# Optimization experiments

Hardware: AMD Instinct MI355X
Metric: run time of the kernel (lower is better)

## Reference

```python
import jax, jax.numpy as jnp
import numpy as np
import math

# dims (see shape_source)
B, S, D, H, DH, W, L, F = 2, 4096, 768, 12, 64, 256, 4, 2048
DV, DID, NIN, V, CD, CS = 256, 32, 8, 4, 16, 64
DEMB = CD * CS
EPS = 1e-6
NEG = -1e9


def rmsnorm(x, w):
    y = x * jax.lax.rsqrt(jnp.mean(x * x, axis=-1, keepdims=True) + EPS)
    return y * w


def sliding_attn(q, k, v):
    # q,k,v: [B,H,S,DH]; banded attention, each query attends keys within +-W.
    nc = S // W
    q = q * (1.0 / math.sqrt(DH))
    kp = jnp.pad(k, ((0, 0), (0, 0), (W, W), (0, 0)))
    vp = jnp.pad(v, ((0, 0), (0, 0), (W, W), (0, 0)))
    idx = jnp.arange(nc)[:, None] * W + jnp.arange(3 * W)[None, :]  # [nc,3W] into padded seq
    kc = kp[:, :, idx]                                # [B,H,nc,3W,DH]
    vc = vp[:, :, idx]
    qc = q.reshape(B, H, nc, W, DH)
    scores = jnp.einsum('bhcqd,bhckd->bhcqk', qc, kc)  # [B,H,nc,W,3W]
    qpos = jnp.arange(W)[:, None]
    kpos = jnp.arange(3 * W)[None, :]
    band = jnp.abs(kpos - (qpos + W)) <= W             # [W,3W]
    kglob = jnp.arange(nc)[:, None, None] * W + kpos[None] - W  # [nc,1,3W]
    valid = band[None] & (kglob >= 0) & (kglob < S)    # [nc,W,3W]
    scores = jnp.where(valid[None, None], scores, NEG)
    probs = jax.nn.softmax(scores, axis=-1)
    out = jnp.einsum('bhcqk,bhckd->bhcqd', probs, vc)
    return out.reshape(B, H, S, DH)


def _forward(x, id, embed_table, cd_w, cd_b, wq, bq, wk, bk, wv, bv,
             attn_norm_w, ffn_norm_w, w1, b1, w2, b2, w3, b3,
             h0_w1, h0_b1, h0_w2, h0_b2, norm_head0_w, head0_w, head0_b,
             c1_w1, c1_b1, c1_w2, c1_b2, c2_w1, c2_b1, c2_w2, c2_b2,
             norm_emb_w, head1_w, head1_b):
    h = embed_table[x] * math.sqrt(DV)                         # [B,S,DV]
    bits = jnp.arange(DID - 1, -1, -1)
    idb = ((id[..., None] >> bits) & 1).astype(jnp.float32)    # decimal2binary -> [B,S,DID]
    h = jnp.concatenate([h, idb], axis=-1) @ cd_w + cd_b       # correct_dim -> [B,S,D]
    for l in range(L):
        a = rmsnorm(h, attn_norm_w[l])
        q = (a @ wq[l] + bq[l]).reshape(B, S, H, DH).transpose(0, 2, 1, 3)
        k = (a @ wk[l] + bk[l]).reshape(B, S, H, DH).transpose(0, 2, 1, 3)
        v = (a @ wv[l] + bv[l]).reshape(B, S, H, DH).transpose(0, 2, 1, 3)
        o = sliding_attn(q, k, v)                              # [B,H,S,DH]
        h = h + o.transpose(0, 2, 1, 3).reshape(B, S, D)
        f = rmsnorm(h, ffn_norm_w[l])
        h = h + (jax.nn.silu(f @ w1[l] + b1[l]) * (f @ w3[l] + b3[l])) @ w2[l] + b2[l]
    # per-token head
    t = jax.nn.silu(h @ h0_w1 + h0_b1) @ h0_w2 + h0_b2
    logits0 = rmsnorm(t, norm_head0_w) @ head0_w + head0_b     # [B,S,V]
    # compression head
    c = jax.nn.silu(h @ c1_w1 + c1_b1) @ c1_w2 + c1_b2         # [B,S,CD]
    c = c.transpose(0, 2, 1)                                    # [B,CD,S]
    c = jax.nn.silu(c @ c2_w1 + c2_b1) @ c2_w2 + c2_b2         # [B,CD,CS]
    c = c.transpose(0, 2, 1).reshape(B, DEMB)
    emb = rmsnorm(c, norm_emb_w)
    logits = (emb @ head1_w + head1_b).reshape(B, S, V)        # [B,S,V]
    return logits0, logits


def setup_inputs() -> dict:
    key = jax.random.key(0)
    ks = iter(jax.random.split(key, 80))
    def w(*shape):
        return jax.random.normal(next(ks), shape, jnp.float32) * 0.02
    z = lambda *shape: jnp.zeros(shape, jnp.float32)
    o = lambda *shape: jnp.ones(shape, jnp.float32)
    return {
        'x': jax.random.randint(next(ks), (B, S), 0, NIN),
        'id': jax.random.randint(next(ks), (B, S), 0, 2 ** 20),
        'embed_table': w(NIN, DV),
        'cd_w': w(DV + DID, D), 'cd_b': z(D),
        'wq': w(L, D, D), 'bq': z(L, D),
        'wk': w(L, D, D), 'bk': z(L, D),
        'wv': w(L, D, D), 'bv': z(L, D),
        'attn_norm_w': o(L, D), 'ffn_norm_w': o(L, D),
        'w1': w(L, D, F), 'b1': z(L, F),
        'w2': w(L, F, D), 'b2': z(L, D),
        'w3': w(L, D, F), 'b3': z(L, F),
        'h0_w1': w(D, D), 'h0_b1': z(D),
        'h0_w2': w(D, D), 'h0_b2': z(D),
        'norm_head0_w': o(D),
        'head0_w': w(D, V), 'head0_b': z(V),
        'c1_w1': w(D, D), 'c1_b1': z(D),
        'c1_w2': w(D, CD), 'c1_b2': z(CD),
        'c2_w1': w(S, S), 'c2_b1': z(S),
        'c2_w2': w(S, CS), 'c2_b2': z(CS),
        'norm_emb_w': o(DEMB),
        'head1_w': w(DEMB, S * V), 'head1_b': z(S * V),
    }


def reference(x, id, embed_table, cd_w, cd_b, wq, bq, wk, bk, wv, bv,
              attn_norm_w, ffn_norm_w, w1, b1, w2, b2, w3, b3,
              h0_w1, h0_b1, h0_w2, h0_b2, norm_head0_w, head0_w, head0_b,
              c1_w1, c1_b1, c1_w2, c1_b2, c2_w1, c2_b1, c2_w2, c2_b2,
              norm_emb_w, head1_w, head1_b):
    return _forward(x, id, embed_table, cd_w, cd_b, wq, bq, wk, bk, wv, bv,
                    attn_norm_w, ffn_norm_w, w1, b1, w2, b2, w3, b3,
                    h0_w1, h0_b1, h0_w2, h0_b2, norm_head0_w, head0_w, head0_b,
                    c1_w1, c1_b1, c1_w2, c1_b2, c2_w1, c2_b1, c2_w2, c2_b2,
                    norm_emb_w, head1_w, head1_b)
```

## Files before the change

kernel.cpp:

```cpp
#include <hip/hip_runtime.h>
#include <stdint.h>

typedef unsigned short u16;
typedef unsigned int u32;

#define SS 4096
#define NROWS 8192

__device__ __forceinline__ float bf2f(u16 u){
  union { u32 u; float f; } x; x.u = ((u32)u) << 16; return x.f;
}
__device__ __forceinline__ u16 f2bf(float f){
  union { float f; u32 u; } x; x.f = f;
  u32 r = x.u + 0x7fffu + ((x.u >> 16) & 1u);
  return (u16)(r >> 16);
}
__device__ __forceinline__ float bflo(u32 u){ union { u32 u; float f; } x; x.u = u << 16; return x.f; }
__device__ __forceinline__ float bfhi(u32 u){ union { u32 u; float f; } x; x.u = u & 0xffff0000u; return x.f; }

__device__ __forceinline__ float ldany(const void* p, size_t i, int f){
  return f ? ((const float*)p)[i] : bf2f(((const u16*)p)[i]);
}

__global__ void detect_k(const void* anw, int* flag){
  if (threadIdx.x == 0 && blockIdx.x == 0)
    flag[0] = (((const u32*)anw)[0] == 0x3F800000u) ? 1 : 0;
}

__device__ __forceinline__ void gload16(const u16* g, u16* l){
  __builtin_amdgcn_global_load_lds((const __attribute__((address_space(1))) void*)g,
                                   (__attribute__((address_space(3))) void*)l, 16, 0, 0);
}

typedef __attribute__((ext_vector_type(8))) __bf16 bf16x8;
typedef __attribute__((ext_vector_type(4))) float f32x4;

__device__ __forceinline__ bf16x8 ldsr16(const u16* p){
  bf16x8 r;
  u32 a = (u32)(uintptr_t)(const __attribute__((address_space(3))) u16*)p;
  asm volatile("ds_read_b128 %0, %1" : "=v"(r) : "v"(a));
  return r;
}

__global__ void transpose_k(const void* __restrict__ in, size_t ioff,
                            u16* __restrict__ out, int R, int C, const int* fl){
  int f = *fl;
  __shared__ u16 t[32][33];
  int c0 = blockIdx.x * 32, r0 = blockIdx.y * 32;
  int tx = threadIdx.x & 31, ty = threadIdx.x >> 5;
  #pragma unroll
  for (int i = 0; i < 32; i += 8){
    int r = r0 + ty + i, c = c0 + tx;
    t[ty + i][tx] = (r < R && c < C) ? f2bf(ldany(in, ioff + (size_t)r * C + c, f)) : (u16)0;
  }
  __syncthreads();
  #pragma unroll
  for (int i = 0; i < 32; i += 8){
    int r = c0 + ty + i, c = r0 + tx;
    if (r < C && c < R) out[(size_t)r * R + c] = t[tx][ty + i];
  }
}

__global__ void transpose_qkv_k(const void* __restrict__ wqp, const void* __restrict__ wkp,
                                const void* __restrict__ wvp, size_t wo,
                                u16* __restrict__ out, const int* fl){
  int f = *fl;
  const void* in = (blockIdx.z == 0) ? wqp : (blockIdx.z == 1) ? wkp : wvp;
  u16* dst = out + (size_t)blockIdx.z * 768 * 768;
  __shared__ u16 t[32][33];
  int c0 = blockIdx.x * 32, r0 = blockIdx.y * 32;
  int tx = threadIdx.x & 31, ty = threadIdx.x >> 5;
  #pragma unroll
  for (int i = 0; i < 32; i += 8){
    int r = r0 + ty + i, c = c0 + tx;
    t[ty + i][tx] = f2bf(ldany(in, wo + (size_t)r * 768 + c, f));
  }
  __syncthreads();
  #pragma unroll
  for (int i = 0; i < 32; i += 8){
    int r = c0 + ty + i, c = r0 + tx;
    dst[(size_t)r * 768 + c] = t[tx][ty + i];
  }
}

__global__ void embed_k(const int* __restrict__ x, const int* __restrict__ idv,
                        const void* __restrict__ table, u16* __restrict__ xin,
                        const int* fl){
  int f = *fl;
  int row = blockIdx.x;
  int tok = x[row], idval = idv[row];
  for (int j = threadIdx.x; j < 288; j += 256){
    u16 o;
    if (j < 256) o = f2bf(ldany(table, (size_t)tok*256 + j, f) * 16.0f);
    else o = ((idval >> (31 - (j - 256))) & 1) ? (u16)0x3F80 : (u16)0;
    xin[(size_t)row * 288 + j] = o;
  }
}

__global__ __launch_bounds__(256) void rmsnormw_k(const u16* __restrict__ in,
                          const void* __restrict__ w, int woff,
                          u16* __restrict__ out, const int* fl){
  int f = *fl;
  int wave = threadIdx.x >> 6, lane = threadIdx.x & 63;
  int row = blockIdx.x*4 + wave;
  const u16* xp = in + (size_t)row * 768;
  float v[12]; float ss = 0.f;
  #pragma unroll
  for (int i = 0; i < 12; ++i){ v[i] = bf2f(xp[i*64 + lane]); ss += v[i]*v[i]; }
  #pragma unroll
  for (int o = 32; o > 0; o >>= 1) ss += __shfl_down(ss, o, 64);
  float tot = __shfl(ss, 0, 64);
  float sc = rsqrtf(tot / 768.f + 1e-6f);
  u16* op = out + (size_t)row * 768;
  #pragma unroll
  for (int i = 0; i < 12; ++i)
    op[i*64 + lane] = f2bf(v[i] * sc * ldany(w, woff + i*64 + lane, f));
}

__global__ void rmsnorm_emb_k(const float* __restrict__ in, const void* __restrict__ b2,
                              const void* __restrict__ w, float* __restrict__ out, const int* fl){
  int f = *fl;
  int row = blockIdx.x;
  const float* xp = in + (size_t)row * 1024;
  float ss = 0.f;
  for (int i = threadIdx.x; i < 1024; i += 256){
    float v = xp[i] + ldany(b2, i >> 4, f); ss += v*v;
  }
  #pragma unroll
  for (int o = 32; o > 0; o >>= 1) ss += __shfl_down(ss, o, 64);
  __shared__ float red[4];
  __shared__ float scale_s;
  int lane = threadIdx.x & 63, wv = threadIdx.x >> 6;
  if (lane == 0) red[wv] = ss;
  __syncthreads();
  if (threadIdx.x == 0){
    float tot = red[0] + red[1] + red[2] + red[3];
    scale_s = rsqrtf(tot / 1024.f + 1e-6f);
  }
  __syncthreads();
  float sc = scale_s;
  for (int i = threadIdx.x; i < 1024; i += 256)
    out[(size_t)row*1024 + i] = (xp[i] + ldany(b2, i >> 4, f)) * sc * ldany(w, i, f);
}

#define BM 128
#define BN 128
#define BK 32
#define GBN 64

__device__ __forceinline__ int xcd_swz(int nwg, int orig){
  int xcd = orig & 7, loc = orig >> 3;
  int q = nwg >> 3, r = nwg & 7;
  return (xcd < r ? xcd * (q + 1) : r * (q + 1) + (xcd - r) * q) + loc;
}

__device__ __forceinline__ int nxt3(int i){ return i == 2 ? 0 : i + 1; }

__global__ __launch_bounds__(256) void gemm_bt_k(
    const u16* __restrict__ A, const u16* __restrict__ BT,
    const void* __restrict__ bias, const void* __restrict__ bias2,
    const void* __restrict__ bias3, int boff,
    u16* __restrict__ out, int M, int N, int K, int epi, const int* fl)
{
  __shared__ u16 As[3][BM*BK];
  __shared__ u16 Bs[3][BN*BK];
  const int tid = threadIdx.x;
  const int wave = tid >> 6, lane = tid & 63;

  const int gx = gridDim.x;
  const int nwg = gx * gridDim.y;
  const int swz = xcd_swz(nwg, blockIdx.y * gx + blockIdx.x);
  const int m0 = (swz / gx) * BM, n0 = (swz % gx) * BN;

  const int wr = (wave >> 1) * 64, wc = (wave & 1) * 64;
  const int lr = lane & 15, lq = lane >> 4;

  f32x4 acc[4][4];
  #pragma unroll
  for (int i = 0; i < 4; ++i)
    #pragma unroll
    for (int j = 0; j < 4; ++j) acc[i][j] = f32x4{0.f,0.f,0.f,0.f};

  const int r_in = lane >> 2;
  const int c_in = (lane & 3) * 8;
  const u16* gA = A  + (size_t)(m0 + wave*32 + r_in) * K + c_in;
  const u16* gB = BT + (size_t)(n0 + wave*32 + r_in) * K + c_in;

  auto stage = [&](int buf, int kt){
    u16* lA = &As[buf][wave*32*BK];
    u16* lB = &Bs[buf][wave*32*BK];
    gload16(gA + kt,        lA);
    gload16(gA + kt + 16*K, lA + 16*BK);
    gload16(gB + kt,        lB);
    gload16(gB + kt + 16*K, lB + 16*BK);
  };

  const int nk = K / BK;
  stage(0, 0);
  stage(1, BK);

  int cur = 0, pre = 2;
  for (int t = 0; t < nk; ++t){
    if (t + 1 < nk) asm volatile("s_waitcnt vmcnt(4)" ::: "memory");
    else            asm volatile("s_waitcnt vmcnt(0)" ::: "memory");
    __builtin_amdgcn_sched_barrier(0);
    __builtin_amdgcn_s_barrier();
    __builtin_amdgcn_sched_barrier(0);
    if (t + 2 < nk) stage(pre, (t + 2) * BK);

    const u16* Ab = &As[cur][0];
    const u16* Bb = &Bs[cur][0];
    bf16x8 af[4], bfr[4];
    #pragma unroll
    for (int i = 0; i < 4; ++i)
      af[i] = ldsr16(Ab + (wr + i*16 + lr) * BK + lq*8);
    #pragma unroll
    for (int j = 0; j < 4; ++j)
      bfr[j] = ldsr16(Bb + (wc + j*16 + lr) * BK + lq*8);
    asm volatile("s_waitcnt lgkmcnt(0)" ::: "memory");
    __builtin_amdgcn_sched_barrier(0);

    __builtin_amdgcn_s_setprio(1);
    #pragma unroll
    for (int i = 0; i < 4; ++i)
      #pragma unroll
      for (int j = 0; j < 4; ++j)
        acc[i][j] = __builtin_amdgcn_mfma_f32_16x16x32_bf16(af[i], bfr[j], acc[i][j], 0, 0, 0);
    __builtin_amdgcn_s_setprio(0);
    __builtin_amdgcn_sched_barrier(0);
    cur = nxt3(cur); pre = nxt3(pre);
  }

  const int f = *fl;
  #pragma unroll
  for (int i = 0; i < 4; ++i){
    #pragma unroll
    for (int j = 0; j < 4; ++j){
      #pragma unroll
      for (int r = 0; r < 4; ++r){
        int row = m0 + wr + i*16 + lq*4 + r;
        int col = n0 + wc + j*16 + lr;
        size_t idx = (size_t)row * N + col;
        float bb;
        if (bias3){
          if (col < 768) bb = ldany(bias, boff + col, f);
          else if (col < 1536) bb = ldany(bias2, boff + col - 768, f);
          else bb = ldany(bias3, boff + col - 1536, f);
        } else {
          bb = ldany(bias, boff + col, f);
        }
        float v = acc[i][j][r] + bb;
        if (epi == 0){
          out[idx] = f2bf(v);
        } else if (epi == 1){
          out[idx] = f2bf(v / (1.f + __expf(-v)));
        } else if (epi == 2){
          float g = bf2f(out[idx]);
          out[idx] = f2bf((g / (1.f + __expf(-g))) * v);
        } else {
          out[idx] = f2bf(bf2f(out[idx]) + v);
        }
      }
    }
  }
}

__global__ __launch_bounds__(256) void gemm_gate_k(
    const u16* __restrict__ A, const u16* __restrict__ B1T, const u16* __restrict__ B3T,
    const void* __restrict__ b1, const void* __restrict__ b3, int boff,
    u16* __restrict__ out, int M, int N, int K, const int* fl)
{
  __shared__ u16 As[3][BM*BK];
  __shared__ u16 B1s[3][GBN*BK];
  __shared__ u16 B3s[3][GBN*BK];
  const int tid = threadIdx.x;
  const int wave = tid >> 6, lane = tid & 63;

  const int gx = gridDim.x;
  const int nwg = gx * gridDim.y;
  const int swz = xcd_swz(nwg, blockIdx.y * gx + blockIdx.x);
  const int m0 = (swz / gx) * BM, n0 = (swz % gx) * GBN;

  const int wr = (wave >> 1) * 64, wc = (wave & 1) * 32;
  const int lr = lane & 15, lq = lane >> 4;

  f32x4 acc1[4][2], acc3[4][2];
  #pragma unroll
  for (int i = 0; i < 4; ++i)
    #pragma unroll
    for (int j = 0; j < 2; ++j){
      acc1[i][j] = f32x4{0.f,0.f,0.f,0.f};
      acc3[i][j] = f32x4{0.f,0.f,0.f,0.f};
    }

  const int r_in = lane >> 2;
  const int c_in = (lane & 3) * 8;
  const u16* gA  = A   + (size_t)(m0 + wave*32 + r_in) * K + c_in;
  const u16* gB1 = B1T + (size_t)(n0 + wave*16 + r_in) * K + c_in;
  const u16* gB3 = B3T + (size_t)(n0 + wave*16 + r_in) * K + c_in;

  auto stage = [&](int buf, int kt){
    gload16(gA + kt,        &As[buf][wave*32*BK]);
    gload16(gA + kt + 16*K, &As[buf][(wave*32 + 16)*BK]);
    gload16(gB1 + kt,       &B1s[buf][wave*16*BK]);
    gload16(gB3 + kt,       &B3s[buf][wave*16*BK]);
  };

  const int nk = K / BK;
  stage(0, 0);
  stage(1, BK);

  int cur = 0, pre = 2;
  for (int t = 0; t < nk; ++t){
    if (t + 1 < nk) asm volatile("s_waitcnt vmcnt(4)" ::: "memory");
    else            asm volatile("s_waitcnt vmcnt(0)" ::: "memory");
    __builtin_amdgcn_sched_barrier(0);
    __builtin_amdgcn_s_barrier();
    __builtin_amdgcn_sched_barrier(0);
    if (t + 2 < nk) stage(pre, (t + 2) * BK);

    const u16* Ab  = &As[cur][0];
    const u16* B1b = &B1s[cur][0];
    const u16* B3b = &B3s[cur][0];
    bf16x8 af[4], b1f[2], b3f[2];
    #pragma unroll
    for (int i = 0; i < 4; ++i)
      af[i] = ldsr16(Ab + (wr + i*16 + lr) * BK + lq*8);
    #pragma unroll
    for (int j = 0; j < 2; ++j){
      b1f[j] = ldsr16(B1b + (wc + j*16 + lr) * BK + lq*8);
      b3f[j] = ldsr16(B3b + (wc + j*16 + lr) * BK + lq*8);
    }
    asm volatile("s_waitcnt lgkmcnt(0)" ::: "memory");
    __builtin_amdgcn_sched_barrier(0);

    __builtin_amdgcn_s_setprio(1);
    #pragma unroll
    for (int i = 0; i < 4; ++i)
      #pragma unroll
      for (int j = 0; j < 2; ++j){
        acc1[i][j] = __builtin_amdgcn_mfma_f32_16x16x32_bf16(af[i], b1f[j], acc1[i][j], 0, 0, 0);
        acc3[i][j] = __builtin_amdgcn_mfma_f32_16x16x32_bf16(af[i], b3f[j], acc3[i][j], 0, 0, 0);
      }
    __builtin_amdgcn_s_setprio(0);
    __builtin_amdgcn_sched_barrier(0);
    cur = nxt3(cur); pre = nxt3(pre);
  }

  const int f = *fl;
  #pragma unroll
  for (int i = 0; i < 4; ++i){
    #pragma unroll
    for (int j = 0; j < 2; ++j){
      #pragma unroll
      for (int r = 0; r < 4; ++r){
        int row = m0 + wr + i*16 + lq*4 + r;
        int col = n0 + wc + j*16 + lr;
        float v1 = acc1[i][j][r] + ldany(b1, boff + col, f);
        float v3 = acc3[i][j][r] + ldany(b3, boff + col, f);
        out[(size_t)row * N + col] = f2bf((v1 / (1.f + __expf(-v1))) * v3);
      }
    }
  }
}

__global__ __launch_bounds__(256) void attn_mfma_k(
    const u16* __restrict__ qkv, u16* __restrict__ h)
{
  __shared__ u16 Ks[64*72];
  __shared__ u16 Vt[64*72];
  __shared__ u16 Pl[4*32*72];
  const int qc = blockIdx.x, hh = blockIdx.y, b = blockIdx.z;
  const int q0 = qc * 128;
  const int tid = threadIdx.x, wave = tid >> 6, lane = tid & 63;
  const int lr = lane & 15, lq = lane >> 4;
  u16* Pw = Pl + wave*32*72;
  const int qrow = q0 + wave*32;

  bf16x8 qf[2][2];
  #pragma unroll
  for (int i = 0; i < 2; ++i)
    #pragma unroll
    for (int kq = 0; kq < 2; ++kq)
      qf[i][kq] = *(const bf16x8*)(qkv + (size_t)(b*SS + qrow + i*16 + lr)*2304 + hh*64 + kq*32 + lq*8);

  float m_r[2][4], l_r[2][4];
  f32x4 acc[2][4];
  #pragma unroll
  for (int i = 0; i < 2; ++i)
    #pragma unroll
    for (int r = 0; r < 4; ++r){ m_r[i][r] = -1e30f; l_r[i][r] = 0.f; }
  #pragma unroll
  for (int i = 0; i < 2; ++i)
    #pragma unroll
    for (int j = 0; j < 4; ++j) acc[i][j] = f32x4{0.f,0.f,0.f,0.f};

  for (int jt = 0; jt < 10; ++jt){
    int t0 = q0 - 256 + jt*64;
    if (t0 + 64 <= 0 || t0 >= SS) continue;

    {
      int n = tid >> 2, dp = (tid & 3) * 16;
      int kg = t0 + n;
      uint4 a = {0,0,0,0}, c = {0,0,0,0};
      if (kg >= 0 && kg < SS){
        const u16* kp = qkv + (size_t)(b*SS+kg)*2304 + 768 + hh*64 + dp;
        a = *(const uint4*)kp; c = *(const uint4*)(kp + 8);
      }
      *(uint4*)(Ks + n*72 + dp)     = a;
      *(uint4*)(Ks + n*72 + dp + 8) = c;
    }
    {
      int n = lane, dp = wave*16;
      int kg = t0 + n;
      uint4 a = {0,0,0,0}, c = {0,0,0,0};
      if (kg >= 0 && kg < SS){
        const u16* vp = qkv + (size_t)(b*SS+kg)*2304 + 1536 + hh*64 + dp;
        a = *(const uint4*)vp; c = *(const uint4*)(vp + 8);
      }
      u32 w[8] = {a.x,a.y,a.z,a.w,c.x,c.y,c.z,c.w};
      #pragma unroll
      for (int e = 0; e < 8; ++e){
        Vt[(dp + e*2    )*72 + n] = (u16)(w[e] & 0xffffu);
        Vt[(dp + e*2 + 1)*72 + n] = (u16)(w[e] >> 16);
      }
    }
    __syncthreads();

    f32x4 sc[2][4];
    #pragma unroll
    for (int i = 0; i < 2; ++i)
      #pragma unroll
      for (int j = 0; j < 4; ++j) sc[i][j] = f32x4{0.f,0.f,0.f,0.f};
    #pragma unroll
    for (int j = 0; j < 4; ++j){
      bf16x8 kfa = *(const bf16x8*)(Ks + (j*16 + lr)*72 + lq*8);
      bf16x8 kfb = *(const bf16x8*)(Ks + (j*16 + lr)*72 + 32 + lq*8);
      #pragma unroll
      for (int i = 0; i < 2; ++i){
        sc[i][j] = __builtin_amdgcn_mfma_f32_16x16x32_bf16(qf[i][0], kfa, sc[i][j], 0, 0, 0);
        sc[i][j] = __builtin_amdgcn_mfma_f32_16x16x32_bf16(qf[i][1], kfb, sc[i][j], 0, 0, 0);
      }
    }

    #pragma unroll
    for (int i = 0; i < 2; ++i){
      #pragma unroll
      for (int r = 0; r < 4; ++r){
        int qg = qrow + i*16 + lq*4 + r;
        #pragma unroll
        for (int j = 0; j < 4; ++j){
          int kg = t0 + j*16 + lr;
          float s = sc[i][j][r] * 0.125f;
          bool ok = (kg >= 0) && (kg < SS) && (kg >= qg - 256) && (kg <= qg + 256);
          sc[i][j][r] = ok ? s : -1e38f;
        }
      }
    }

    #pragma unroll
    for (int i = 0; i < 2; ++i){
      #pragma unroll
      for (int r = 0; r < 4; ++r){
        float mx = fmaxf(fmaxf(sc[i][0][r], sc[i][1][r]), fmaxf(sc[i][2][r], sc[i][3][r]));
        #pragma unroll
        for (int o = 1; o < 16; o <<= 1) mx = fmaxf(mx, __shfl_xor(mx, o, 64));
        float mn = fmaxf(m_r[i][r], mx);
        float al = __expf(m_r[i][r] - mn);
        float ps = 0.f;
        #pragma unroll
        for (int j = 0; j < 4; ++j){
          float p = __expf(sc[i][j][r] - mn);
          sc[i][j][r] = p; ps += p;
        }
        #pragma unroll
        for (int o = 1; o < 16; o <<= 1) ps += __shfl_xor(ps, o, 64);
        l_r[i][r] = l_r[i][r] * al + ps;
        m_r[i][r] = mn;
        #pragma unroll
        for (int j = 0; j < 4; ++j) acc[i][j][r] *= al;
      }
    }

    #pragma unroll
    for (int i = 0; i < 2; ++i)
      #pragma unroll
      for (int j = 0; j < 4; ++j)
        #pragma unroll
        for (int r = 0; r < 4; ++r)
          Pw[(i*16 + lq*4 + r)*72 + j*16 + lr] = f2bf(sc[i][j][r]);

    #pragma unroll
    for (int kq = 0; kq < 2; ++kq){
      bf16x8 pf0 = *(const bf16x8*)(Pw + lr*72        + kq*32 + lq*8);
      bf16x8 pf1 = *(const bf16x8*)(Pw + (16 + lr)*72 + kq*32 + lq*8);
      #pragma unroll
      for (int j = 0; j < 4; ++j){
        bf16x8 vfj = *(const bf16x8*)(Vt + (j*16 + lr)*72 + kq*32 + lq*8);
        acc[0][j] = __builtin_amdgcn_mfma_f32_16x16x32_bf16(pf0, vfj, acc[0][j], 0, 0, 0);
        acc[1][j] = __builtin_amdgcn_mfma_f32_16x16x32_bf16(pf1, vfj, acc[1][j], 0, 0, 0);
      }
    }
    __syncthreads();
  }

  #pragma unroll
  for (int i = 0; i < 2; ++i){
    #pragma unroll
    for (int r = 0; r < 4; ++r){
      float inv = 1.f / l_r[i][r];
      int qg = qrow + i*16 + lq*4 + r;
      u16* hp = h + (size_t)(b*SS + qg)*768 + hh*64;
      #pragma unroll
      for (int j = 0; j < 4; ++j){
        int d = j*16 + lr;
        hp[d] = f2bf(bf2f(hp[d]) + acc[i][j][r] * inv);
      }
    }
  }
}

template<int NN>
__global__ __launch_bounds__(256) void smalln_k(const u16* __restrict__ A, const void* __restrict__ W,
                         const void* __restrict__ bias, void* __restrict__ out,
                         const int* fl, int outmode){
  int f = *fl;
  __shared__ float Wl[NN*768];
  for (int i = threadIdx.x; i < NN*768; i += 256){
    int n = i / 768, k = i - n*768;
    Wl[i] = ldany(W, (size_t)k*NN + n, f);
  }
  __syncthreads();
  int wave = threadIdx.x >> 6, lane = threadIdx.x & 63;
  int rowbase = blockIdx.x*16 + wave*4;
  for (int r = 0; r < 4; ++r){
    int row = rowbase + r;
    const u16* ap = A + (size_t)row * 768;
    float a[12];
    #pragma unroll
    for (int i = 0; i < 12; ++i) a[i] = bf2f(ap[i*64 + lane]);
    float acc[NN];
    #pragma unroll
    for (int n = 0; n < NN; ++n) acc[n] = 0.f;
    #pragma unroll
    for (int i = 0; i < 12; ++i){
      int k = i*64 + lane;
      #pragma unroll
      for (int n = 0; n < NN; ++n) acc[n] += a[i] * Wl[n*768 + k];
    }
    float red[NN];
    #pragma unroll
    for (int n = 0; n < NN; ++n){
      float v = acc[n];
      #pragma unroll
      for (int o = 32; o > 0; o >>= 1) v += __shfl_down(v, o, 64);
      red[n] = v;
    }
    if (lane == 0){
      #pragma unroll
      for (int n = 0; n < NN; ++n){
        float v = red[n] + ldany(bias, n, f);
        size_t oi = (size_t)row*NN + n;
        if (outmode && f) ((float*)out)[oi] = v;
        else ((u16*)out)[oi] = f2bf(v);
      }
    }
  }
}

__global__ void ctrans_k(const u16* __restrict__ in, u16* __restrict__ out){
  int idx = blockIdx.x * 256 + threadIdx.x;
  int b = idx >> 16;
  int r = idx & 65535;
  int d = r >> 12, s = r & 4095;
  out[idx] = in[(size_t)(b*4096 + s)*16 + d];
}

__global__ __launch_bounds__(256) void c2mlp1_k(const u16* __restrict__ ct,
    const void* __restrict__ w, float* __restrict__ yacc, const int* fl){
  int f = *fl;
  __shared__ float Awt[64][36];
  __shared__ u16 Ws[64*128];
  int n0 = blockIdx.x * 128;
  int k0 = blockIdx.y * 512;
  int tid = threadIdx.x;
  int c4 = (tid & 31) * 4;
  int r0 = (tid >> 5) * 4;
  float acc[4][4] = {};
  for (int ks = 0; ks < 512; ks += 64){
    __syncthreads();
    {
      int mm = tid >> 3, kk8 = (tid & 7) * 8;
      uint4 av = *(const uint4*)(ct + (size_t)mm*4096 + k0 + ks + kk8);
      float fv[8] = {bflo(av.x),bfhi(av.x),bflo(av.y),bfhi(av.y),
                     bflo(av.z),bfhi(av.z),bflo(av.w),bfhi(av.w)};
      #pragma unroll
      for (int i = 0; i < 8; ++i) Awt[kk8+i][mm] = fv[i];
    }
    {
      int kk = tid >> 2, cc = (tid & 3) * 32;
      #pragma unroll
      for (int j = 0; j < 32; ++j)
        Ws[kk*128 + cc + j] = f2bf(ldany(w, (size_t)(k0+ks+kk)*4096 + n0 + cc + j, f));
    }
    __syncthreads();
    for (int kk = 0; kk < 64; ++kk){
      float4 a4 = *(const float4*)&Awt[kk][r0];
      uint2 wv = *(const uint2*)(Ws + kk*128 + c4);
      float w0 = bflo(wv.x), w1v = bfhi(wv.x), w2v = bflo(wv.y), w3v = bfhi(wv.y);
      float ar[4] = {a4.x, a4.y, a4.z, a4.w};
      #pragma unroll
      for (int r = 0; r < 4; ++r){
        acc[r][0] += ar[r]*w0;  acc[r][1] += ar[r]*w1v;
        acc[r][2] += ar[r]*w2v; acc[r][3] += ar[r]*w3v;
      }
    }
  }
  #pragma unroll
  for (int r = 0; r < 4; ++r)
    #pragma unroll
    for (int cc = 0; cc < 4; ++cc)
      atomicAdd(&yacc[(size_t)(r0+r)*4096 + n0 + c4 + cc], acc[r][cc]);
}

__global__ void silu_bias_k(const float* __restrict__ yacc, const void* __restrict__ bias,
                            u16* __restrict__ out, const int* fl){
  int f = *fl;
  int idx = blockIdx.x*256 + threadIdx.x;
  int n = idx & 4095;
  float v = yacc[idx] + ldany(bias, n, f);
  out[idx] = f2bf(v / (1.f + __expf(-v)));
}

__global__ void c2mlp2_k(const u16* __restrict__ y, const void* __restrict__ w2,
                         float* __restrict__ emb_pre, const int* fl){
  int f = *fl;
  int m = blockIdx.x, kseg = blockIdx.y;
  int col = threadIdx.x & 63, sl = threadIdx.x >> 6;
  float acc = 0.f;
  int kb = kseg*512 + sl*128;
  for (int k = kb; k < kb+128; ++k)
    acc += bf2f(y[(size_t)m*4096 + k]) * ldany(w2, (size_t)k*64 + col, f);
  __shared__ float red[256];
  red[threadIdx.x] = acc;
  __syncthreads();
  if (sl == 0){
    float t = red[col] + red[col+64] + red[col+128] + red[col+192];
    int b = m >> 4, d = m & 15;
    atomicAdd(&emb_pre[b*1024 + col*16 + d], t);
  }
}

__global__ void head1_k(const float* __restrict__ emb, const void* __restrict__ w,
                        float* __restrict__ hacc, const int* fl){
  int f = *fl;
  int n = blockIdx.x*256 + threadIdx.x;
  int k0 = blockIdx.y*256;
  float a0 = 0.f, a1 = 0.f;
  for (int k = k0; k < k0+256; ++k){
    float wv = ldany(w, (size_t)k*16384 + n, f);
    a0 += emb[k] * wv;
    a1 += emb[1024 + k] * wv;
  }
  atomicAdd(&hacc[n], a0);
  atomicAdd(&hacc[16384 + n], a1);
}

__global__ void head1fin_k(const float* __restrict__ hacc, const void* __restrict__ bias,
                           void* __restrict__ out, const int* fl){
  int f = *fl;
  int n = blockIdx.x*256 + threadIdx.x;
  float b = ldany(bias, n, f);
  float a0 = hacc[n] + b, a1 = hacc[16384 + n] + b;
  if (f){ ((float*)out)[32768 + n] = a0; ((float*)out)[49152 + n] = a1; }
  else  { ((u16*)out)[32768 + n] = f2bf(a0); ((u16*)out)[49152 + n] = f2bf(a1); }
}

extern "C" void kernel_launch(void* const* d_in, const int* in_sizes, int n_in,
                              void* d_out, int out_size, void* d_ws, size_t ws_size,
                              hipStream_t stream)
{
  const int* x   = (const int*)d_in[0];
  const int* idv = (const int*)d_in[1];
  const void* embt = d_in[2];
  const void* cd_w = d_in[3];
  const void* cd_b = d_in[4];
  const void* wq = d_in[5];
  const void* bq = d_in[6];
  const void* wk = d_in[7];
  const void* bk = d_in[8];
  const void* wv = d_in[9];
  const void* bv = d_in[10];
  const void* attn_nw = d_in[11];
  const void* ffn_nw  = d_in[12];
  const void* w1 = d_in[13];
  const void* b1 = d_in[14];
  const void* w2 = d_in[15];
  const void* b2 = d_in[16];
  const void* w3 = d_in[17];
  const void* b3 = d_in[18];
  const void* h0_w1 = d_in[19];
  const void* h0_b1 = d_in[20];
  const void* h0_w2 = d_in[21];
  const void* h0_b2 = d_in[22];
  const void* nh0_w = d_in[23];
  const void* head0_w = d_in[24];
  const void* head0_b = d_in[25];
  const void* c1_w1 = d_in[26];
  const void* c1_b1 = d_in[27];
  const void* c1_w2 = d_in[28];
  const void* c1_b2 = d_in[29];
  const void* c2_w1 = d_in[30];
  const void* c2_b1 = d_in[31];
  const void* c2_w2 = d_in[32];
  const void* c2_b2 = d_in[33];
  const void* nemb_w = d_in[34];
  const void* head1_w = d_in[35];
  const void* head1_b = d_in[36];

  char* ws = (char*)d_ws;
  size_t off = 0;
  auto alloc = [&](size_t bytes)->char*{
    char* p = ws + off; off = (off + bytes + 255) & ~(size_t)255; return p;
  };

  int*  flag  = (int*)alloc(256);
  u16*  wtbuf = (u16*)alloc((size_t)(2304+2048)*768*2);
  u16*  wt2nd = wtbuf + (size_t)2048*768;
  u16*  h     = (u16*)alloc((size_t)NROWS*768*2);
  u16*  fbuf  = (u16*)alloc((size_t)NROWS*768*2);
  char* R3    = alloc((size_t)NROWS*768*2*3);

  u16* xin  = (u16*)R3;
  u16* qkvb = (u16*)R3;
  u16* g1   = (u16*)R3;
  u16* tbuf = (u16*)R3;
  u16* gbuf = (u16*)(R3 + (size_t)NROWS*768*2);
  char* tail = R3 + (size_t)NROWS*768*2*2;
  u16* cbuf = (u16*)tail;
  u16* ctb  = (u16*)(tail + 262144);
  float* yacc = (float*)(tail + 262144*2);
  u16* ybf  = (u16*)(tail + 262144*2 + 524288);
  float* emb_pre = (float*)(tail + 262144*3 + 524288);
  float* embn    = (float*)(tail + 262144*3 + 524288 + 8192);
  float* hacc    = (float*)(tail + 262144*3 + 524288 + 16384);

  detect_k<<<1, 64, 0, stream>>>(attn_nw, flag);

  auto tr = [&](const void* src, size_t ioff, u16* dst, int R, int C){
    dim3 g((C+31)/32, (R+31)/32);
    transpose_k<<<g, 256, 0, stream>>>(src, ioff, dst, R, C, flag);
  };
  auto gemm = [&](const u16* A, const u16* BT, const void* bias, int boff,
                  u16* out_, int M, int N, int K, int epi){
    dim3 g(N/128, M/128);
    gemm_bt_k<<<g, 256, 0, stream>>>(A, BT, bias, nullptr, nullptr, boff,
                                     out_, M, N, K, epi, flag);
  };

  embed_k<<<NROWS, 256, 0, stream>>>(x, idv, embt, xin, flag);
  tr(cd_w, 0, wtbuf, 288, 768);
  gemm(xin, wtbuf, cd_b, 0, h, NROWS, 768, 288, 0);

  for (int l = 0; l < 4; ++l){
    size_t wo = (size_t)l*768*768, fo = (size_t)l*768*2048;
    rmsnormw_k<<<NROWS/4, 256, 0, stream>>>(h, attn_nw, l*768, fbuf, flag);
    transpose_qkv_k<<<dim3(24,24,3), 256, 0, stream>>>(wq, wk, wv, wo, wtbuf, flag);
    {
      dim3 g(2304/128, NROWS/128);
      gemm_bt_k<<<g, 256, 0, stream>>>(fbuf, wtbuf, bq, bk, bv, l*768,
                                       qkvb, NROWS, 2304, 768, 0, flag);
    }
    attn_mfma_k<<<dim3(32,12,2), 256, 0, stream>>>(qkvb, h);

    rmsnormw_k<<<NROWS/4, 256, 0, stream>>>(h, ffn_nw, l*768, fbuf, flag);
    tr(w1, fo, wtbuf, 768, 2048);
    tr(w3, fo, wt2nd, 768, 2048);
    {
      dim3 g(2048/GBN, NROWS/128);
      gemm_gate_k<<<g, 256, 0, stream>>>(fbuf, wtbuf, wt2nd, b1, b3, l*2048,
                                         g1, NROWS, 2048, 768, flag);
    }
    tr(w2, fo, wtbuf, 2048, 768);
    gemm(g1, wtbuf, b2, l*768, h, NROWS, 768, 2048, 3);
  }

  tr(h0_w1, 0, wtbuf, 768, 768);
  gemm(h, wtbuf, h0_b1, 0, gbuf, NROWS, 768, 768, 1);
  tr(h0_w2, 0, wtbuf, 768, 768);
  gemm(gbuf, wtbuf, h0_b2, 0, tbuf, NROWS, 768, 768, 0);
  rmsnormw_k<<<NROWS/4, 256, 0, stream>>>(tbuf, nh0_w, 0, gbuf, flag);
  smalln_k<4><<<NROWS/16, 256, 0, stream>>>(gbuf, head0_w, head0_b, d_out, flag, 1);

  tr(c1_w1, 0, wtbuf, 768, 768);
  gemm(h, wtbuf, c1_b1, 0, gbuf, NROWS, 768, 768, 1);
  smalln_k<16><<<NROWS/16, 256, 0, stream>>>(gbuf, c1_w2, c1_b2, cbuf, flag, 0);
  ctrans_k<<<512, 256, 0, stream>>>(cbuf, ctb);
  hipMemsetAsync(yacc, 0, (size_t)32*4096*4, stream);
  hipMemsetAsync(emb_pre, 0, 2*1024*4, stream);
  hipMemsetAsync(hacc, 0, (size_t)2*16384*4, stream);
  c2mlp1_k<<<dim3(32,8), 256, 0, stream>>>(ctb, c2_w1, yacc, flag);
  silu_bias_k<<<512, 256, 0, stream>>>(yacc, c2_b1, ybf, flag);
  c2mlp2_k<<<dim3(32,8), 256, 0, stream>>>(ybf, c2_w2, emb_pre, flag);
  rmsnorm_emb_k<<<2, 256, 0, stream>>>(emb_pre, c2_b2, nemb_w, embn, flag);
  head1_k<<<dim3(64,4), 256, 0, stream>>>(embn, head1_w, hacc, flag);
  head1fin_k<<<64, 256, 0, stream>>>(hacc, head1_b, d_out, flag);

  (void)in_sizes; (void)n_in; (void)out_size; (void)ws_size;
}
```

Baseline: 1.952 ms.

## Stage GEMM and attention epilogues through LDS for vectorized stores; split LDS waits

The GEMM, gated-GEMM and attention kernels now write their output tiles to shared memory first. They then emit 16-byte coalesced global loads and stores instead of scattered 2-byte stores, and the residual add and gate read-modify-writes are vectorized the same way. The main GEMM loops also issue LDS fragment loads in a staggered order with partial lgkmcnt waits, so MFMAs on the first row fragment can start before all fragments arrive. This adds an extra LDS pass and barriers in the epilogue, and it rounds to bf16 once more before the residual add.

```diff
diff --git a/kernel.cpp b/kernel.cpp
--- a/kernel.cpp
+++ b/kernel.cpp
@@ -162,8 +162,9 @@
     const void* __restrict__ bias3, int boff,
     u16* __restrict__ out, int M, int N, int K, int epi, const int* fl)
 {
-  __shared__ u16 As[3][BM*BK];
-  __shared__ u16 Bs[3][BN*BK];
+  __shared__ u16 pool[24576];
+  u16* As = pool;
+  u16* Bs = pool + 3*BM*BK;
   const int tid = threadIdx.x;
   const int wave = tid >> 6, lane = tid & 63;
 
@@ -187,8 +188,8 @@
   const u16* gB = BT + (size_t)(n0 + wave*32 + r_in) * K + c_in;
 
   auto stage = [&](int buf, int kt){
-    u16* lA = &As[buf][wave*32*BK];
-    u16* lB = &Bs[buf][wave*32*BK];
+    u16* lA = As + buf*BM*BK + wave*32*BK;
+    u16* lB = Bs + buf*BN*BK + wave*32*BK;
     gload16(gA + kt,        lA);
     gload16(gA + kt + 16*K, lA + 16*BK);
     gload16(gB + kt,        lB);
@@ -208,59 +209,91 @@
     __builtin_amdgcn_sched_barrier(0);
     if (t + 2 < nk) stage(pre, (t + 2) * BK);
 
-    const u16* Ab = &As[cur][0];
-    const u16* Bb = &Bs[cur][0];
+    const u16* Ab = As + cur*BM*BK;
+    const u16* Bb = Bs + cur*BN*BK;
     bf16x8 af[4], bfr[4];
-    #pragma unroll
-    for (int i = 0; i < 4; ++i)
-      af[i] = ldsr16(Ab + (wr + i*16 + lr) * BK + lq*8);
+    af[0] = ldsr16(Ab + (wr + lr) * BK + lq*8);
     #pragma unroll
     for (int j = 0; j < 4; ++j)
       bfr[j] = ldsr16(Bb + (wc + j*16 + lr) * BK + lq*8);
+    #pragma unroll
+    for (int i = 1; i < 4; ++i)
+      af[i] = ldsr16(Ab + (wr + i*16 + lr) * BK + lq*8);
+
+    __builtin_amdgcn_s_setprio(1);
+    asm volatile("s_waitcnt lgkmcnt(3)" ::: "memory");
+    __builtin_amdgcn_sched_barrier(0);
+    #pragma unroll
+    for (int j = 0; j < 4; ++j)
+      acc[0][j] = __builtin_amdgcn_mfma_f32_16x16x32_bf16(af[0], bfr[j], acc[0][j], 0, 0, 0);
+    asm volatile("s_waitcnt lgkmcnt(2)" ::: "memory");
+    __builtin_amdgcn_sched_barrier(0);
+    #pragma unroll
+    for (int j = 0; j < 4; ++j)
+      acc[1][j] = __builtin_amdgcn_mfma_f32_16x16x32_bf16(af[1], bfr[j], acc[1][j], 0, 0, 0);
+    asm volatile("s_waitcnt lgkmcnt(1)" ::: "memory");
+    __builtin_amdgcn_sched_barrier(0);
+    #pragma unroll
+    for (int j = 0; j < 4; ++j)
+      acc[2][j] = __builtin_amdgcn_mfma_f32_16x16x32_bf16(af[2], bfr[j], acc[2][j], 0, 0, 0);
     asm volatile("s_waitcnt lgkmcnt(0)" ::: "memory");
     __builtin_amdgcn_sched_barrier(0);
-
-    __builtin_amdgcn_s_setprio(1);
-    #pragma unroll
-    for (int i = 0; i < 4; ++i)
-      #pragma unroll
-      for (int j = 0; j < 4; ++j)
-        acc[i][j] = __builtin_amdgcn_mfma_f32_16x16x32_bf16(af[i], bfr[j], acc[i][j], 0, 0, 0);
+    #pragma unroll
+    for (int j = 0; j < 4; ++j)
+      acc[3][j] = __builtin_amdgcn_mfma_f32_16x16x32_bf16(af[3], bfr[j], acc[3][j], 0, 0, 0);
     __builtin_amdgcn_s_setprio(0);
     __builtin_amdgcn_sched_barrier(0);
     cur = nxt3(cur); pre = nxt3(pre);
   }
 
   const int f = *fl;
+  __syncthreads();
+  u16* T = pool;
   #pragma unroll
   for (int i = 0; i < 4; ++i){
     #pragma unroll
     for (int j = 0; j < 4; ++j){
       #pragma unroll
       for (int r = 0; r < 4; ++r){
-        int row = m0 + wr + i*16 + lq*4 + r;
-        int col = n0 + wc + j*16 + lr;
-        size_t idx = (size_t)row * N + col;
+        int row = wr + i*16 + lq*4 + r;
+        int col = wc + j*16 + lr;
+        int gcol = n0 + col;
         float bb;
         if (bias3){
-          if (col < 768) bb = ldany(bias, boff + col, f);
-          else if (col < 1536) bb = ldany(bias2, boff + col - 768, f);
-          else bb = ldany(bias3, boff + col - 1536, f);
+          if (gcol < 768) bb = ldany(bias, boff + gcol, f);
+          else if (gcol < 1536) bb = ldany(bias2, boff + gcol - 768, f);
+          else bb = ldany(bias3, boff + gcol - 1536, f);
         } else {
-          bb = ldany(bias, boff + col, f);
+          bb = ldany(bias, boff + gcol, f);
         }
         float v = acc[i][j][r] + bb;
-        if (epi == 0){
-          out[idx] = f2bf(v);
-        } else if (epi == 1){
-          out[idx] = f2bf(v / (1.f + __expf(-v)));
-        } else if (epi == 2){
-          float g = bf2f(out[idx]);
-          out[idx] = f2bf((g / (1.f + __expf(-g))) * v);
-        } else {
-          out[idx] = f2bf(bf2f(out[idx]) + v);
-        }
-      }
+        u16 o;
+        if (epi == 1) o = f2bf(v / (1.f + __expf(-v)));
+        else          o = f2bf(v);
+        T[row*136 + col] = o;
+      }
+    }
+  }
+  __syncthreads();
+  #pragma unroll
+  for (int it = 0; it < 8; ++it){
+    int id = it*256 + tid;
+    int row = id >> 4, c = id & 15;
+    uint4 v = *(const uint4*)(T + row*136 + c*8);
+    size_t gidx = (size_t)(m0 + row) * N + n0 + c*8;
+    if (epi == 2 || epi == 3){
+      uint4 g = *(const uint4*)(out + gidx);
+      const u16* vp = (const u16*)&v; const u16* gp = (const u16*)&g;
+      uint4 o; u16* op = (u16*)&o;
+      #pragma unroll
+      for (int e = 0; e < 8; ++e){
+        float vv = bf2f(vp[e]), gg = bf2f(gp[e]);
+        op[e] = (epi == 3) ? f2bf(gg + vv)
+                           : f2bf((gg / (1.f + __expf(-gg))) * vv);
+      }
+      *(uint4*)(out + gidx) = o;
+    } else {
+      *(uint4*)(out + gidx) = v;
     }
   }
 }
@@ -270,9 +303,10 @@
     const void* __restrict__ b1, const void* __restrict__ b3, int boff,
     u16* __restrict__ out, int M, int N, int K, const int* fl)
 {
-  __shared__ u16 As[3][BM*BK];
-  __shared__ u16 B1s[3][GBN*BK];
-  __shared__ u16 B3s[3][GBN*BK];
+  __shared__ u16 pool[24576];
+  u16* As  = pool;
+  u16* B1s = pool + 3*BM*BK;
+  u16* B3s = pool + 3*BM*BK + 3*GBN*BK;
   const int tid = threadIdx.x;
   const int wave = tid >> 6, lane = tid & 63;
 
@@ -300,10 +334,10 @@
   const u16* gB3 = B3T + (size_t)(n0 + wave*16 + r_in) * K + c_in;
 
   auto stage = [&](int buf, int kt){
-    gload16(gA + kt,        &As[buf][wave*32*BK]);
-    gload16(gA + kt + 16*K, &As[buf][(wave*32 + 16)*BK]);
-    gload16(gB1 + kt,       &B1s[buf][wave*16*BK]);
-    gload16(gB3 + kt,       &B3s[buf][wave*16*BK]);
+    gload16(gA + kt,        As + buf*BM*BK + wave*32*BK);
+    gload16(gA + kt + 16*K, As + buf*BM*BK + (wave*32 + 16)*BK);
+    gload16(gB1 + kt,       B1s + buf*GBN*BK + wave*16*BK);
+    gload16(gB3 + kt,       B3s + buf*GBN*BK + wave*16*BK);
   };
 
   const int nk = K / BK;
@@ -319,57 +353,88 @@
     __builtin_amdgcn_sched_barrier(0);
     if (t + 2 < nk) stage(pre, (t + 2) * BK);
 
-    const u16* Ab  = &As[cur][0];
-    const u16* B1b = &B1s[cur][0];
-    const u16* B3b = &B3s[cur][0];
+    const u16* Ab  = As  + cur*BM*BK;
+    const u16* B1b = B1s + cur*GBN*BK;
+    const u16* B3b = B3s + cur*GBN*BK;
     bf16x8 af[4], b1f[2], b3f[2];
-    #pragma unroll
-    for (int i = 0; i < 4; ++i)
-      af[i] = ldsr16(Ab + (wr + i*16 + lr) * BK + lq*8);
+    af[0] = ldsr16(Ab + (wr + lr) * BK + lq*8);
     #pragma unroll
     for (int j = 0; j < 2; ++j){
       b1f[j] = ldsr16(B1b + (wc + j*16 + lr) * BK + lq*8);
       b3f[j] = ldsr16(B3b + (wc + j*16 + lr) * BK + lq*8);
     }
+    #pragma unroll
+    for (int i = 1; i < 4; ++i)
+      af[i] = ldsr16(Ab + (wr + i*16 + lr) * BK + lq*8);
+
+    __builtin_amdgcn_s_setprio(1);
+    asm volatile("s_waitcnt lgkmcnt(3)" ::: "memory");
+    __builtin_amdgcn_sched_barrier(0);
+    #pragma unroll
+    for (int j = 0; j < 2; ++j){
+      acc1[0][j] = __builtin_amdgcn_mfma_f32_16x16x32_bf16(af[0], b1f[j], acc1[0][j], 0, 0, 0);
+      acc3[0][j] = __builtin_amdgcn_mfma_f32_16x16x32_bf16(af[0], b3f[j], acc3[0][j], 0, 0, 0);
+    }
+    asm volatile("s_waitcnt lgkmcnt(2)" ::: "memory");
+    __builtin_amdgcn_sched_barrier(0);
+    #pragma unroll
+    for (int j = 0; j < 2; ++j){
+      acc1[1][j] = __builtin_amdgcn_mfma_f32_16x16x32_bf16(af[1], b1f[j], acc1[1][j], 0, 0, 0);
+      acc3[1][j] = __builtin_amdgcn_mfma_f32_16x16x32_bf16(af[1], b3f[j], acc3[1][j], 0, 0, 0);
+    }
+    asm volatile("s_waitcnt lgkmcnt(1)" ::: "memory");
+    __builtin_amdgcn_sched_barrier(0);
+    #pragma unroll
+    for (int j = 0; j < 2; ++j){
+      acc1[2][j] = __builtin_amdgcn_mfma_f32_16x16x32_bf16(af[2], b1f[j], acc1[2][j], 0, 0, 0);
+      acc3[2][j] = __builtin_amdgcn_mfma_f32_16x16x32_bf16(af[2], b3f[j], acc3[2][j], 0, 0, 0);
+    }
     asm volatile("s_waitcnt lgkmcnt(0)" ::: "memory");
     __builtin_amdgcn_sched_barrier(0);
-
-    __builtin_amdgcn_s_setprio(1);
-    #pragma unroll
-    for (int i = 0; i < 4; ++i)
-      #pragma unroll
-      for (int j = 0; j < 2; ++j){
-        acc1[i][j] = __builtin_amdgcn_mfma_f32_16x16x32_bf16(af[i], b1f[j], acc1[i][j], 0, 0, 0);
-        acc3[i][j] = __builtin_amdgcn_mfma_f32_16x16x32_bf16(af[i], b3f[j], acc3[i][j], 0, 0, 0);
-      }
+    #pragma unroll
+    for (int j = 0; j < 2; ++j){
+      acc1[3][j] = __builtin_amdgcn_mfma_f32_16x16x32_bf16(af[3], b1f[j], acc1[3][j], 0, 0, 0);
+      acc3[3][j] = __builtin_amdgcn_mfma_f32_16x16x32_bf16(af[3], b3f[j], acc3[3][j], 0, 0, 0);
+    }
     __builtin_amdgcn_s_setprio(0);
     __builtin_amdgcn_sched_barrier(0);
     cur = nxt3(cur); pre = nxt3(pre);
   }
 
   const int f = *fl;
+  __syncthreads();
+  u16* T = pool;
   #pragma unroll
   for (int i = 0; i < 4; ++i){
     #pragma unroll
     for (int j = 0; j < 2; ++j){
       #pragma unroll
       for (int r = 0; r < 4; ++r){
-        int row = m0 + wr + i*16 + lq*4 + r;
-        int col = n0 + wc + j*16 + lr;
-        float v1 = acc1[i][j][r] + ldany(b1, boff + col, f);
-        float v3 = acc3[i][j][r] + ldany(b3, boff + col, f);
-        out[(size_t)row * N + col] = f2bf((v1 / (1.f + __expf(-v1))) * v3);
-      }
-    }
+        int row = wr + i*16 + lq*4 + r;
+        int col = wc + j*16 + lr;
+        float v1 = acc1[i][j][r] + ldany(b1, boff + n0 + col, f);
+        float v3 = acc3[i][j][r] + ldany(b3, boff + n0 + col, f);
+        T[row*72 + col] = f2bf((v1 / (1.f + __expf(-v1))) * v3);
+      }
+    }
+  }
+  __syncthreads();
+  #pragma unroll
+  for (int it = 0; it < 4; ++it){
+    int id = it*256 + tid;
+    int row = id >> 3, c = id & 7;
+    uint4 v = *(const uint4*)(T + row*72 + c*8);
+    *(uint4*)(out + (size_t)(m0 + row) * N + n0 + c*8) = v;
   }
 }
 
 __global__ __launch_bounds__(256) void attn_mfma_k(
     const u16* __restrict__ qkv, u16* __restrict__ h)
 {
-  __shared__ u16 Ks[64*72];
-  __shared__ u16 Vt[64*72];
-  __shared__ u16 Pl[4*32*72];
+  __shared__ u16 pool[18432];
+  u16* Ks = pool;
+  u16* Vt = pool + 4608;
+  u16* Pl = pool + 9216;
   const int qc = blockIdx.x, hh = blockIdx.y, b = blockIdx.z;
   const int q0 = qc * 128;
   const int tid = threadIdx.x, wave = tid >> 6, lane = tid & 63;
@@ -504,19 +569,32 @@
     __syncthreads();
   }
 
+  u16* T = pool;
   #pragma unroll
   for (int i = 0; i < 2; ++i){
     #pragma unroll
     for (int r = 0; r < 4; ++r){
       float inv = 1.f / l_r[i][r];
-      int qg = qrow + i*16 + lq*4 + r;
-      u16* hp = h + (size_t)(b*SS + qg)*768 + hh*64;
-      #pragma unroll
-      for (int j = 0; j < 4; ++j){
-        int d = j*16 + lr;
-        hp[d] = f2bf(bf2f(hp[d]) + acc[i][j][r] * inv);
-      }
-    }
+      int row = wave*32 + i*16 + lq*4 + r;
+      #pragma unroll
+      for (int j = 0; j < 4; ++j)
+        T[row*72 + j*16 + lr] = f2bf(acc[i][j][r] * inv);
+    }
+  }
+  __syncthreads();
+  #pragma unroll
+  for (int it = 0; it < 4; ++it){
+    int id = it*256 + tid;
+    int row = id >> 3, c = id & 7;
+    u16* hp = h + (size_t)(b*SS + q0 + row)*768 + hh*64 + c*8;
+    uint4 g = *(const uint4*)hp;
+    uint4 v = *(const uint4*)(T + row*72 + c*8);
+    const u16* gp = (const u16*)&g; const u16* vp = (const u16*)&v;
+    uint4 o; u16* op = (u16*)&o;
+    #pragma unroll
+    for (int e = 0; e < 8; ++e)
+      op[e] = f2bf(bf2f(gp[e]) + bf2f(vp[e]));
+    *(uint4*)hp = o;
   }
 }
 
```

After: 1.794 ms. -8.1%, faster.
